# Optimization experiments

Measured on AMD Instinct MI355X. Metric: run time of the kernel, lower is better.

## Reference

```python
import jax, jax.numpy as jnp
import numpy as np

B, L, D = 8, 2048, 512


def setup_inputs() -> dict:
    key = jax.random.key(0)
    ks = jax.random.split(key, 9)
    s = 1.0 / np.sqrt(D)
    x = jax.random.normal(ks[0], (B, L, D), dtype=jnp.float32)
    Wq = jax.random.uniform(ks[1], (D, D), jnp.float32, -s, s)
    bq = jax.random.uniform(ks[2], (D,), jnp.float32, -s, s)
    Wk = jax.random.uniform(ks[3], (D, D), jnp.float32, -s, s)
    bk = jax.random.uniform(ks[4], (D,), jnp.float32, -s, s)
    Wv = jax.random.uniform(ks[5], (D, D), jnp.float32, -s, s)
    bv = jax.random.uniform(ks[6], (D,), jnp.float32, -s, s)
    Wo = jax.random.uniform(ks[7], (D, D), jnp.float32, -s, s)
    bo = jax.random.uniform(ks[8], (D,), jnp.float32, -s, s)
    return {"x": x, "Wq": Wq, "bq": bq, "Wk": Wk, "bk": bk,
            "Wv": Wv, "bv": bv, "Wo": Wo, "bo": bo}


def reference(x, Wq, bq, Wk, bk, Wv, bv, Wo, bo):
    # Projections then rfft along sequence axis -> complex [B, F, D], F = L//2+1
    Q = jnp.fft.rfft(x @ Wq + bq, axis=1)
    K = jnp.fft.rfft(x @ Wk + bk, axis=1)
    V = jnp.fft.rfft(x @ Wv + bv, axis=1)
    scale = K.shape[-1] ** (-0.5)
    # Complex attention scores over frequency bins: [B, F, F]
    att = jnp.einsum('bfd,bgd->bfg', Q, K) * scale
    attn = jax.nn.softmax(jnp.abs(att), axis=-1)
    context = jnp.einsum('bfg,bgd->bfd', attn.astype(Q.dtype), V)
    context = jnp.fft.irfft(context, n=x.shape[1], axis=1)  # [B, L, D] real
    return context @ Wo + bo
```

## Files before the change

### kernel.cpp

```cpp
#include <hip/hip_runtime.h>
#include <hip/hip_bf16.h>
#include <math.h>

typedef __hip_bfloat16 bf16;
typedef __attribute__((ext_vector_type(8))) short short8;
typedef __attribute__((ext_vector_type(4))) float f32x4;

#define BB 8
#define LL 2048
#define DD 512
#define FF 1025
#define GP 1088
#define FPAD 1152
#define PSTRIDE 589824
#define ATT_SCALE 0.04419417382415922f

__device__ __forceinline__ float b2f(bf16 v) { return __bfloat162float(v); }
__device__ __forceinline__ bf16  f2b(float v) { return __float2bfloat16(v); }
__device__ __forceinline__ float s2f(short s) { bf16 t; *reinterpret_cast<short*>(&t) = s; return b2f(t); }
__device__ __forceinline__ unsigned pk2f(float a, float b) {
    bf16 ha = f2b(a), hb = f2b(b);
    return (unsigned)*(unsigned short*)&ha | ((unsigned)*(unsigned short*)&hb << 16);
}

#define MFMA16(a, b, c) __builtin_amdgcn_mfma_f32_16x16x32_bf16((a), (b), (c), 0, 0, 0)

__device__ __forceinline__ short8 neg8(short8 v) {
    short8 r;
    #pragma unroll
    for (int t = 0; t < 8; ++t) r[t] = (short)(v[t] ^ (short)0x8000);
    return r;
}

typedef __attribute__((address_space(1))) const unsigned int gu32;
typedef __attribute__((address_space(3))) unsigned int lu32;
__device__ __forceinline__ void gl16(const void* g, void* l) {
    __builtin_amdgcn_global_load_lds((gu32*)g, (lu32*)l, 16, 0, 0);
}

template<bool F32>
__device__ __forceinline__ float ldin(const void* p, size_t i) {
    if (F32) return ((const float*)p)[i];
    else     return b2f(((const bf16*)p)[i]);
}

__global__ __launch_bounds__(256) void detect_dtype(const unsigned short* __restrict__ x,
                                                    int* __restrict__ flag)
{
    __shared__ int cnt[256];
    int c = 0;
    for (int i = threadIdx.x; i < 4096; i += 256) {
        const int e = (x[i] >> 7) & 0xFF;
        c += (e >= 100 && e <= 150) ? 1 : 0;
    }
    cnt[threadIdx.x] = c;
    __syncthreads();
    for (int s = 128; s; s >>= 1) {
        if (threadIdx.x < s) cnt[threadIdx.x] += cnt[threadIdx.x + s];
        __syncthreads();
    }
    if (threadIdx.x == 0) *flag = (cnt[0] < 3400) ? 1 : 0;
}

__global__ __launch_bounds__(256) void prep_bias(const void* __restrict__ b0,
                                                 const void* __restrict__ b1,
                                                 const void* __restrict__ b2,
                                                 const void* __restrict__ b3,
                                                 float* __restrict__ bias_f,
                                                 const int* __restrict__ flag)
{
    const int idx = blockIdx.x * 256 + threadIdx.x;
    const int which = idx >> 9, i = idx & 511;
    const void* src = which == 0 ? b0 : (which == 1 ? b1 : (which == 2 ? b2 : b3));
    bias_f[idx] = (*flag) ? ldin<true>(src, i) : ldin<false>(src, i);
}

__global__ __launch_bounds__(256) void split_w_t(const void* __restrict__ W0,
                                                 const void* __restrict__ W1,
                                                 const void* __restrict__ W2,
                                                 const void* __restrict__ W3,
                                                 bf16* __restrict__ WT,
                                                 const int* __restrict__ flag)
{
    const int z = blockIdx.z;
    const void* W = z == 0 ? W0 : (z == 1 ? W1 : (z == 2 ? W2 : W3));
    bf16* Wh = WT + (size_t)z * 524288;
    const int k0 = blockIdx.x * 32, n0 = blockIdx.y * 32;
    const bool f32 = (*flag) != 0;
    __shared__ float Tl[32][33];
    for (int it = 0; it < 4; ++it) {
        const int idx = it * 256 + threadIdx.x;
        const int lk = idx >> 5, ln = idx & 31;
        Tl[lk][ln] = f32 ? ldin<true>(W, (size_t)(k0 + lk) * 512 + n0 + ln)
                         : ldin<false>(W, (size_t)(k0 + lk) * 512 + n0 + ln);
    }
    __syncthreads();
    for (int it = 0; it < 4; ++it) {
        const int idx = it * 256 + threadIdx.x;
        const int ln = idx >> 5, lk = idx & 31;
        Wh[(size_t)(n0 + ln) * 512 + k0 + lk] = f2b(Tl[lk][ln]);
    }
}

__device__ __forceinline__ int shx(int i, int c) {
    const int x = (i << 2) | c;
    return x ^ (((x >> 6) & 3) << 2);
}

__device__ __forceinline__ void fft_decode(int flat, int& b, int& dp) {
    const int c8 = flat & 7;
    const int s  = (flat >> 3) & 1;
    const int pp = flat >> 4;
    const int idx = c8 * 32 + pp;
    b  = idx >> 5;
    dp = ((idx & 31) << 1) | s;
}

__device__ __forceinline__ void fill_twl(float2* twl, int tid) {
    for (int idx = tid; idx < 2047; idx += 512) {
        const int l2 = 31 - __builtin_clz((unsigned)(2047 - idx));
        const int m = 1 << l2;
        const int k = idx - 2048 + 2 * m;
        float s, c2;
        __sincosf(-3.14159265358979f * (float)k / (float)m, &s, &c2);
        twl[idx] = make_float2(c2, s);
    }
}

__global__ __launch_bounds__(512) void rfft_x(const void* __restrict__ x,
                                              bf16* __restrict__ Xh,
                                              const int* __restrict__ flag)
{
    int b, dp;
    fft_decode(blockIdx.x, b, dp);
    const int d0 = dp * 8;
    __shared__ float2 sh[8192];
    __shared__ float2 twl[2048];
    const int tid = threadIdx.x;
    const int c = tid & 3;

    if (*flag) {
        const float* base = (const float*)x + (size_t)b * 2048 * 512 + d0;
        #pragma unroll
        for (int it = 0; it < 8; ++it) {
            const int idx = it * 512 + tid;
            const int l = idx >> 1, fq = idx & 1;
            const float4 v = *(const float4*)(base + (size_t)l * 512 + fq * 4);
            sh[shx(l, fq * 2)]     = make_float2(v.x, v.y);
            sh[shx(l, fq * 2 + 1)] = make_float2(v.z, v.w);
        }
    } else {
        const bf16* base = (const bf16*)x + (size_t)b * 2048 * 512 + d0;
        #pragma unroll
        for (int it = 0; it < 4; ++it) {
            const int l = it * 512 + tid;
            const short8 v = *(const short8*)(base + (size_t)l * 512);
            #pragma unroll
            for (int q = 0; q < 4; ++q)
                sh[shx(l, q)] = make_float2(s2f(v[2 * q]), s2f(v[2 * q + 1]));
        }
    }
    fill_twl(twl, tid);
    __syncthreads();

    const int jb = tid >> 2;
    #pragma unroll
    for (int lsm = 10; lsm >= 0; --lsm) {
        const int m = 1 << lsm;
        const int base = 2048 - (m << 1);
        #pragma unroll
        for (int r = 0; r < 8; ++r) {
            const int j  = jb + 128 * r;
            const int k  = j & (m - 1);
            const int i1 = ((j & ~(m - 1)) << 1) | k;
            const int i2 = i1 + m;
            const float2 w = twl[base + k];
            const float cw = w.x, sw = w.y;
            const float2 a  = sh[shx(i1, c)];
            const float2 bb = sh[shx(i2, c)];
            sh[shx(i1, c)] = make_float2(a.x + bb.x, a.y + bb.y);
            const float dx = a.x - bb.x, dy = a.y - bb.y;
            sh[shx(i2, c)] = make_float2(dx * cw - dy * sw, dx * sw + dy * cw);
        }
        __syncthreads();
    }

    const int fb = tid >> 2;
    const size_t pan_re = (size_t)(b * 64 + dp) * FPAD;
    const size_t pan_im = pan_re + (size_t)512 * FPAD;
    auto dorow = [&](int f) {
        const int rf = __brev((unsigned)f) >> 21;
        const int rc = __brev((unsigned)((2048 - f) & 2047)) >> 21;
        const float2 Zf = sh[shx(rf, c)];
        const float2 Zc = sh[shx(rc, c)];
        const float x1r = 0.5f * (Zf.x + Zc.x);
        const float x1i = 0.5f * (Zf.y - Zc.y);
        const float x2r = 0.5f * (Zf.y + Zc.y);
        const float x2i = -0.5f * (Zf.x - Zc.x);
        const size_t ro_re = (pan_re + f) * 8 + 2 * c;
        const size_t ro_im = (pan_im + f) * 8 + 2 * c;
        *(unsigned*)&Xh[ro_re] = pk2f(x1r, x2r);
        *(unsigned*)&Xh[ro_im] = pk2f(x1i, x2i);
    };
    #pragma unroll
    for (int it = 0; it < 8; ++it)
        dorow(fb * 8 + it);
    if (tid < 4) dorow(1024);

    if (tid < 254) {
        const int f = FF + (tid >> 1);
        const int w = tid & 1;
        const size_t off = (((size_t)(w * 512 + b * 64 + dp)) * FPAD + f) * 8;
        short8 z = {};
        *(short8*)&Xh[off] = z;
    }
}

__global__ __launch_bounds__(256, 2) void proj_all(const bf16* __restrict__ Xh,
                                                   const bf16* __restrict__ WT,
                                                   const float* __restrict__ bias_f,
                                                   bf16* __restrict__ Q,
                                                   bf16* __restrict__ K,
                                                   bf16* __restrict__ Vct)
{
    const int flat = blockIdx.x;
    const bool isV = flat < 576;
    int t, ny, z;
    if (isV) { t = flat >> 2; ny = flat & 3; z = 2; }
    else { const int idx = flat - 576; t = idx >> 3; z = (idx >> 2) & 1; ny = idx & 3; }

    const int pb = t / 9;
    const int f0 = (t - pb * 9) * 128;
    const int plane = pb >> 3, b = pb & 7;
    const int n0 = ny * 128;
    const int tid = threadIdx.x, wv = tid >> 6, lane = tid & 63;
    const int wm = (wv >> 1) * 64, wn = (wv & 1) * 64;
    const size_t pbase = (size_t)pb * PSTRIDE;

    const bf16* Bh = WT + (size_t)z * 524288;
    const float* bias = bias_f + z * 512;

    __shared__ __align__(1024) bf16 SH[32768];

    const int r8 = lane >> 3;
    const int sl = lane & 7;
    const int q  = sl ^ r8;
    const int r16 = lane & 15, cc = lane >> 4;
    const int rs8 = r16 & 7;
    const int nn2 = lane & 15, rq = (lane >> 4) * 4;

    auto STAGE = [&](int buf, int kt) {
        char* base = (char*)SH + buf * 32768;
        #pragma unroll
        for (int c2 = 0; c2 < 4; ++c2) {
            const int chunk = wv * 4 + c2;
            const int row = chunk * 8 + r8;
            gl16(&Xh[pbase + ((size_t)((kt >> 3) + q) * FPAD + f0 + row) * 8],
                 base + chunk * 1024);
            gl16(&Bh[(size_t)(n0 + row) * 512 + kt + q * 8],
                 base + 16384 + chunk * 1024);
        }
    };

    f32x4 acc[4][4] = {};
    STAGE(0, 0);
    for (int it = 0; it < 8; ++it) {
        if (it < 7) {
            STAGE((it + 1) & 1, (it + 1) * 64);
            asm volatile("s_waitcnt vmcnt(8)" ::: "memory");
        } else {
            asm volatile("s_waitcnt vmcnt(0)" ::: "memory");
        }
        __builtin_amdgcn_s_barrier();
        __builtin_amdgcn_sched_barrier(0);

        const bf16* Ab = SH + (it & 1) * 16384;
        const bf16* Bb = Ab + 8192;
        #pragma unroll
        for (int kk = 0; kk < 2; ++kk) {
            short8 af[4], bfr[4];
            const int sa = ((kk * 4 + cc) ^ rs8) * 8;
            #pragma unroll
            for (int i = 0; i < 4; ++i) {
                af[i]  = *(const short8*)&Ab[(wm + i * 16 + r16) * 64 + sa];
                bfr[i] = *(const short8*)&Bb[(wn + i * 16 + r16) * 64 + sa];
            }
            #pragma unroll
            for (int i = 0; i < 4; ++i)
                #pragma unroll
                for (int j = 0; j < 4; ++j)
                    acc[i][j] = MFMA16(af[i], bfr[j], acc[i][j]);
        }
        asm volatile("s_waitcnt lgkmcnt(0)" ::: "memory");
        __builtin_amdgcn_s_barrier();
    }

    if (!isV) {
        bf16* dst = z == 0 ? Q : K;
        const size_t SPQ = (size_t)BB * FF * DD;
        #pragma unroll
        for (int i = 0; i < 4; ++i)
            #pragma unroll
            for (int j = 0; j < 4; ++j) {
                const int col = n0 + wn + j * 16 + nn2;
                #pragma unroll
                for (int r = 0; r < 4; ++r) {
                    const int f = f0 + wm + i * 16 + rq + r;
                    if (f < FF) {
                        float v = acc[i][j][r];
                        if (plane == 0 && f == 0) v += 2048.0f * bias[col];
                        const int swz = ((f >> 1) & 3) << 3;
                        dst[(size_t)plane * SPQ + ((size_t)(b * FF + f)) * 512 + (col ^ swz)] = f2b(v);
                    }
                }
            }
    } else {
        bf16* T = SH;
        #pragma unroll
        for (int i = 0; i < 4; ++i)
            #pragma unroll
            for (int j = 0; j < 4; ++j) {
                const int col_l = wn + j * 16 + nn2;
                #pragma unroll
                for (int r = 0; r < 4; ++r) {
                    const int row_l = wm + i * 16 + rq + r;
                    const int f = f0 + row_l;
                    float v = (f < FF) ? acc[i][j][r] : 0.f;
                    if (plane == 0 && f == 0) v += 2048.0f * bias[n0 + col_l];
                    T[col_l * 128 + (row_l ^ ((col_l & 15) << 3))] = f2b(v);
                }
            }
        __syncthreads();

        const int nl = tid >> 1, half = tid & 1;
        const size_t gbase = ((size_t)(b * 1024 + plane * 512 + n0 + nl)) * GP + f0;
        #pragma unroll
        for (int a = 0; a < 8; ++a) {
            const int fl = half * 64 + a * 8;
            if (f0 + fl < GP) {
                const short8 v8 = *(const short8*)&T[nl * 128 + (fl ^ ((nl & 15) << 3))];
                *(short8*)&Vct[gbase + fl] = v8;
            }
        }
    }
}

__global__ __launch_bounds__(256, 2) void att_mfma(const bf16* __restrict__ Asp,
                                                   const bf16* __restrict__ Bsp,
                                                   float* __restrict__ att)
{
    const size_t SP = (size_t)BB * FF * DD;
    const int flat = blockIdx.x;
    const int b    = flat & 7;
    const int slot = flat >> 3;
    const int grp  = slot / 51;
    const int rem  = slot % 51;
    const int g    = rem / 3;
    const int r3   = rem % 3;
    const int ft   = grp * 3 + r3;
    const int f0 = ft * 128, g0 = g * 64;

    const int tid = threadIdx.x;
    const int wv = tid >> 6, lane = tid & 63;
    const int wvf = wv >> 1, wvg = wv & 1;

    __shared__ __align__(1024) char LB[49152];

    f32x4 accr[4][2] = {}; f32x4 acci[4][2] = {};

    const int r16 = lane & 15, cc = lane >> 4;
    const int rpos = (cc ^ ((r16 >> 1) & 3)) * 8;
    const size_t abase = (size_t)(b * FF + f0) * 512;
    const size_t bbase = (size_t)(b * FF + g0) * 512;
    const int lrow = lane >> 2;
    const int lcol = (lane & 3) * 8;

    for (int kt = 0; kt < 512; kt += 64) {
        #pragma unroll
        for (int c2 = 0; c2 < 8; ++c2) {
            const int chunk = wv * 8 + c2;
            const int half = chunk >> 4;
            const int pl = (chunk >> 3) & 1, rg = chunk & 7;
            const int row = rg * 16 + lrow;
            gl16(&Asp[(size_t)pl * SP + abase + (size_t)row * 512 + kt + half * 32 + lcol],
                 LB + half * 16384 + ((pl << 3) | rg) * 1024);
        }
        #pragma unroll
        for (int c2 = 0; c2 < 4; ++c2) {
            const int chunk = wv * 4 + c2;
            const int half = chunk >> 3;
            const int pl = (chunk >> 2) & 1, rg = chunk & 3;
            const int row = rg * 16 + lrow;
            gl16(&Bsp[(size_t)pl * SP + bbase + (size_t)row * 512 + kt + half * 32 + lcol],
                 LB + 32768 + half * 8192 + ((pl << 2) | rg) * 1024);
        }
        __syncthreads();

        #pragma unroll
        for (int kk = 0; kk < 2; ++kk) {
            bf16 (*Al)[128][32] = (bf16(*)[128][32])(LB + kk * 16384);
            bf16 (*Bl)[64][32]  = (bf16(*)[64][32])(LB + 32768 + kk * 8192);
            short8 aA[4][2], bB[2][2], nb[2];
            #pragma unroll
            for (int i = 0; i < 4; ++i) {
                const int row = wvf * 64 + i * 16 + r16;
                #pragma unroll
                for (int pl = 0; pl < 2; ++pl)
                    aA[i][pl] = *(const short8*)&Al[pl][row][rpos];
            }
            #pragma unroll
            for (int j = 0; j < 2; ++j) {
                const int row = wvg * 32 + j * 16 + r16;
                #pragma unroll
                for (int pl = 0; pl < 2; ++pl)
                    bB[j][pl] = *(const short8*)&Bl[pl][row][rpos];
                nb[j] = neg8(bB[j][1]);
            }
            #pragma unroll
            for (int i = 0; i < 4; ++i)
                #pragma unroll
                for (int j = 0; j < 2; ++j) {
                    accr[i][j] = MFMA16(aA[i][0], bB[j][0], accr[i][j]);
                    accr[i][j] = MFMA16(aA[i][1], nb[j],    accr[i][j]);
                    acci[i][j] = MFMA16(aA[i][0], bB[j][1], acci[i][j]);
                    acci[i][j] = MFMA16(aA[i][1], bB[j][0], acci[i][j]);
                }
        }
        __syncthreads();
    }

    const int rq = (lane >> 4) * 4;
    #pragma unroll
    for (int i = 0; i < 4; ++i)
        #pragma unroll
        for (int j = 0; j < 2; ++j)
            #pragma unroll
            for (int r = 0; r < 4; ++r) {
                const int f = f0 + wvf * 64 + i * 16 + rq + r;
                const int gg = g0 + wvg * 32 + j * 16 + r16;
                if (f < FF && gg < FF) {
                    const float ar = accr[i][j][r];
                    const float ai = acci[i][j][r];
                    att[((size_t)(b * FF + f)) * FF + gg] = ATT_SCALE * sqrtf(ar * ar + ai * ai);
                }
            }
}

__global__ __launch_bounds__(256) void softmax_rows(const float* __restrict__ att,
                                                    bf16* __restrict__ att16)
{
    const int row = blockIdx.x;
    const float* p = att + (size_t)row * FF;
    bf16* q = att16 + (size_t)row * GP;
    const int tid = threadIdx.x;
    const int lane = tid & 63, wid = tid >> 6;
    __shared__ float srow[1028];
    __shared__ float red[4];

    float m = -1e30f;
    for (int i = tid; i < FF; i += 256) {
        const float v = p[i];
        srow[i] = v;
        m = fmaxf(m, v);
    }
    #pragma unroll
    for (int o = 32; o; o >>= 1) m = fmaxf(m, __shfl_down(m, o));
    if (lane == 0) red[wid] = m;
    __syncthreads();
    m = fmaxf(fmaxf(red[0], red[1]), fmaxf(red[2], red[3]));
    __syncthreads();

    float s = 0.f;
    for (int i = tid; i < FF; i += 256) {
        const float e = expf(srow[i] - m);
        srow[i] = e;
        s += e;
    }
    #pragma unroll
    for (int o = 32; o; o >>= 1) s += __shfl_down(s, o);
    if (lane == 0) red[wid] = s;
    __syncthreads();
    s = red[0] + red[1] + red[2] + red[3];
    const float inv = 1.f / s;
    for (int i = tid; i < GP; i += 256)
        q[i] = f2b(i < FF ? srow[i] * inv : 0.f);
}

__global__ __launch_bounds__(256, 2) void ctx_mfma(const bf16* __restrict__ att16,
                                                   const bf16* __restrict__ Vct,
                                                   bf16* __restrict__ Csp)
{
    const int flat = blockIdx.x;
    const int b    = flat & 7;
    const int slot = flat >> 3;
    const int ft   = slot >> 4;
    const int nt   = slot & 15;
    const int f0 = ft * 128, n0 = nt * 64;

    const int tid = threadIdx.x;
    const int wv = tid >> 6, lane = tid & 63;
    const int wvf = wv >> 1, wvg = wv & 1;

    __shared__ __align__(1024) bf16 SH[24576];

    f32x4 acc[4][2] = {};
    const int r8 = lane >> 3, sl = lane & 7, q = sl ^ r8;
    const int r16 = lane & 15, cc = lane >> 4;
    const int rs8 = r16 & 7;

    auto STAGE = [&](int buf, int kt) {
        char* base = (char*)SH + buf * 24576;
        #pragma unroll
        for (int c2 = 0; c2 < 4; ++c2) {
            const int chunk = wv * 4 + c2;
            const int row = chunk * 8 + r8;
            gl16(&att16[((size_t)(b * FF + f0 + row)) * GP + kt + q * 8],
                 base + chunk * 1024);
        }
        #pragma unroll
        for (int c2 = 0; c2 < 2; ++c2) {
            const int chunk = wv * 2 + c2;
            const int row = chunk * 8 + r8;
            gl16(&Vct[((size_t)(b * 1024 + n0 + row)) * GP + kt + q * 8],
                 base + 16384 + chunk * 1024);
        }
    };

    STAGE(0, 0);
    for (int it = 0; it < 17; ++it) {
        if (it < 16) {
            STAGE((it + 1) & 1, (it + 1) * 64);
            asm volatile("s_waitcnt vmcnt(6)" ::: "memory");
        } else {
            asm volatile("s_waitcnt vmcnt(0)" ::: "memory");
        }
        __builtin_amdgcn_s_barrier();
        __builtin_amdgcn_sched_barrier(0);

        const bf16* Ab = SH + (it & 1) * 12288;
        const bf16* Bb = Ab + 8192;
        #pragma unroll
        for (int kk = 0; kk < 2; ++kk) {
            short8 aA[4], bB[2];
            const int sa = ((kk * 4 + cc) ^ rs8) * 8;
            #pragma unroll
            for (int i = 0; i < 4; ++i)
                aA[i] = *(const short8*)&Ab[(wvf * 64 + i * 16 + r16) * 64 + sa];
            #pragma unroll
            for (int j = 0; j < 2; ++j)
                bB[j] = *(const short8*)&Bb[(wvg * 32 + j * 16 + r16) * 64 + sa];
            #pragma unroll
            for (int i = 0; i < 4; ++i)
                #pragma unroll
                for (int j = 0; j < 2; ++j)
                    acc[i][j] = MFMA16(aA[i], bB[j], acc[i][j]);
        }
        asm volatile("s_waitcnt lgkmcnt(0)" ::: "memory");
        __builtin_amdgcn_s_barrier();
    }

    const int rq = (lane >> 4) * 4;
    #pragma unroll
    for (int i = 0; i < 4; ++i)
        #pragma unroll
        for (int j = 0; j < 2; ++j)
            #pragma unroll
            for (int r = 0; r < 4; ++r) {
                const int f = f0 + wvf * 64 + i * 16 + rq + r;
                const int n = n0 + wvg * 32 + j * 16 + r16;
                if (f < FF) {
                    const int d = n & 511, pl = n >> 9;
                    Csp[((size_t)(pl * 8 + b) * FPAD + f) * 512 + d] = f2b(acc[i][j][r]);
                }
            }
}

__global__ __launch_bounds__(256, 2) void out_mfma_freq(const bf16* __restrict__ A,
                                                        const bf16* __restrict__ BhT,
                                                        float* __restrict__ CwR,
                                                        float* __restrict__ CwI)
{
    const int t = blockIdx.x;
    const int pb = t / 9;
    const int f0 = (t - pb * 9) * 128;
    const int plane = pb >> 3, b = pb & 7;
    const int m0 = t * 128, n0 = blockIdx.y * 64;
    const int tid = threadIdx.x, wv = tid >> 6, lane = tid & 63;
    const int wvf = wv >> 1, wvg = wv & 1;

    __shared__ __align__(1024) bf16 SH[24576];

    f32x4 acc[4][2] = {};
    const int r8 = lane >> 3, sl = lane & 7, q = sl ^ r8;
    const int r16 = lane & 15, cc = lane >> 4;
    const int rs8 = r16 & 7;

    auto STAGE = [&](int buf, int kt) {
        char* base = (char*)SH + buf * 24576;
        #pragma unroll
        for (int c2 = 0; c2 < 4; ++c2) {
            const int chunk = wv * 4 + c2;
            const int row = chunk * 8 + r8;
            gl16(&A[(size_t)(m0 + row) * 512 + kt + q * 8],
                 base + chunk * 1024);
        }
        #pragma unroll
        for (int c2 = 0; c2 < 2; ++c2) {
            const int chunk = wv * 2 + c2;
            const int row = chunk * 8 + r8;
            gl16(&BhT[(size_t)(n0 + row) * 512 + kt + q * 8],
                 base + 16384 + chunk * 1024);
        }
    };

    STAGE(0, 0);
    for (int it = 0; it < 8; ++it) {
        if (it < 7) {
            STAGE((it + 1) & 1, (it + 1) * 64);
            asm volatile("s_waitcnt vmcnt(6)" ::: "memory");
        } else {
            asm volatile("s_waitcnt vmcnt(0)" ::: "memory");
        }
        __builtin_amdgcn_s_barrier();
        __builtin_amdgcn_sched_barrier(0);

        const bf16* Ab = SH + (it & 1) * 12288;
        const bf16* Bb = Ab + 8192;
        #pragma unroll
        for (int kk = 0; kk < 2; ++kk) {
            short8 af[4], bfr[2];
            const int sa = ((kk * 4 + cc) ^ rs8) * 8;
            #pragma unroll
            for (int i = 0; i < 4; ++i)
                af[i] = *(const short8*)&Ab[(wvf * 64 + i * 16 + r16) * 64 + sa];
            #pragma unroll
            for (int j = 0; j < 2; ++j)
                bfr[j] = *(const short8*)&Bb[(wvg * 32 + j * 16 + r16) * 64 + sa];
            #pragma unroll
            for (int i = 0; i < 4; ++i)
                #pragma unroll
                for (int j = 0; j < 2; ++j)
                    acc[i][j] = MFMA16(af[i], bfr[j], acc[i][j]);
        }
        asm volatile("s_waitcnt lgkmcnt(0)" ::: "memory");
        __builtin_amdgcn_s_barrier();
    }

    float* dst = plane ? CwI : CwR;
    const int nn2 = lane & 15, rq = (lane >> 4) * 4;
    #pragma unroll
    for (int i = 0; i < 4; ++i)
        #pragma unroll
        for (int j = 0; j < 2; ++j) {
            const int col = n0 + wvg * 32 + j * 16 + nn2;
            #pragma unroll
            for (int r = 0; r < 4; ++r) {
                const int f = f0 + wvf * 64 + i * 16 + rq + r;
                if (f < FF)
                    dst[((size_t)(b * FF + f)) * 512 + col] = acc[i][j][r];
            }
        }
}

__global__ __launch_bounds__(512) void irfft8(const float* __restrict__ CwR,
                                              const float* __restrict__ CwI,
                                              void* __restrict__ out,
                                              const float* __restrict__ bias_f,
                                              const int* __restrict__ flag)
{
    int b, dp;
    fft_decode(blockIdx.x, b, dp);
    const int d0 = dp * 8;
    __shared__ float2 sh[8192];
    __shared__ float2 twl[2048];
    const int tid = threadIdx.x;
    const int c = tid & 3, fb = tid >> 2;

    for (int it = 0; it < 9; ++it) {
        const int f = fb + 128 * it;
        if (f < FF) {
            const size_t off = ((size_t)(b * FF + f)) * 512 + d0 + 2 * c;
            const float2 vr = *(const float2*)(CwR + off);
            const float2 vi = *(const float2*)(CwI + off);
            float c1x = vr.x, c1y = vi.x, c2x = vr.y, c2y = vi.y;
            if (f == 0 || f == 1024) { c1y = 0.f; c2y = 0.f; }
            sh[shx(f, c)] = make_float2(c1x - c2y, c1y + c2x);
            if (f >= 1 && f <= 1023)
                sh[shx(2048 - f, c)] = make_float2(c1x + c2y, c2x - c1y);
        }
    }
    fill_twl(twl, tid);
    __syncthreads();

    const int jb = fb;
    #pragma unroll
    for (int lsm = 10; lsm >= 0; --lsm) {
        const int m = 1 << lsm;
        const int base = 2048 - (m << 1);
        #pragma unroll
        for (int r = 0; r < 8; ++r) {
            const int j  = jb + 128 * r;
            const int k  = j & (m - 1);
            const int i1 = ((j & ~(m - 1)) << 1) | k;
            const int i2 = i1 + m;
            const float2 w = twl[base + k];
            const float cw = w.x, sw = -w.y;
            const float2 a  = sh[shx(i1, c)];
            const float2 bb = sh[shx(i2, c)];
            sh[shx(i1, c)] = make_float2(a.x + bb.x, a.y + bb.y);
            const float dx = a.x - bb.x, dy = a.y - bb.y;
            sh[shx(i2, c)] = make_float2(dx * cw - dy * sw, dx * sw + dy * cw);
        }
        __syncthreads();
    }

    const float sc = 1.0f / 2048.0f;
    const float bo0 = bias_f[1536 + d0 + 2 * c];
    const float bo1 = bias_f[1536 + d0 + 2 * c + 1];
    const bool f32o = (*flag) != 0;
    const int lb = tid >> 2;
    #pragma unroll
    for (int it = 0; it < 16; ++it) {
        const int l  = lb * 16 + it;
        const int rl = __brev((unsigned)l) >> 21;
        const float2 z = sh[shx(rl, c)];
        const float o0 = z.x * sc + bo0;
        const float o1 = z.y * sc + bo1;
        const size_t off = ((size_t)(b * 2048 + l)) * 512 + d0 + 2 * c;
        if (f32o) {
            *(float2*)((float*)out + off) = make_float2(o0, o1);
        } else {
            __hip_bfloat162 h;
            h.x = f2b(o0); h.y = f2b(o1);
            *(__hip_bfloat162*)((bf16*)out + off) = h;
        }
    }
}

extern "C" void kernel_launch(void* const* d_in, const int* in_sizes, int n_in,
                              void* d_out, int out_size, void* d_ws, size_t ws_size,
                              hipStream_t stream)
{
    const void* x  = d_in[0];
    const void* Wq = d_in[1]; const void* bq = d_in[2];
    const void* Wk = d_in[3]; const void* bk = d_in[4];
    const void* Wv = d_in[5]; const void* bv = d_in[6];
    const void* Wo = d_in[7]; const void* bo = d_in[8];

    char* ws = (char*)d_ws;
    char* pA = ws;
    char* pB = pA + 33652736;
    char* pC = pB + 37748736;
    char* pD = pC + 17039360;
    char* pE = pD + 17039360;
    char* pW = pE + 17825792;

    float*  attn = (float*)pA;
    bf16*   Xh   = (bf16*)pB;
    bf16*   att16= (bf16*)pB;
    bf16*   Csp  = (bf16*)(pB + 17843200);
    bf16*   Asp  = (bf16*)pC;
    bf16*   Bsp  = (bf16*)pD;
    float*  CwR  = (float*)pC;
    float*  CwI  = (float*)pD;
    bf16*   Vct  = (bf16*)pE;
    bf16*   WT   = (bf16*)pW;
    float*  bias_f = (float*)(pW + 4194304);
    int*    flag = (int*)(pW + 4194304 + 8192);

    detect_dtype<<<1, 256, 0, stream>>>((const unsigned short*)x, flag);
    prep_bias<<<8, 256, 0, stream>>>(bq, bk, bv, bo, bias_f, flag);
    split_w_t<<<dim3(16, 16, 4), 256, 0, stream>>>(Wq, Wk, Wv, Wo, WT, flag);
    rfft_x<<<dim3(512), 512, 0, stream>>>(x, Xh, flag);
    proj_all<<<dim3(1728), 256, 0, stream>>>(Xh, WT, bias_f, Asp, Bsp, Vct);
    att_mfma<<<dim3(1224), 256, 0, stream>>>(Asp, Bsp, attn);
    softmax_rows<<<dim3(BB * FF), 256, 0, stream>>>(attn, att16);
    ctx_mfma<<<dim3(1152), 256, 0, stream>>>(att16, Vct, Csp);
    out_mfma_freq<<<dim3(144, 8), 256, 0, stream>>>(Csp, WT + 3 * 524288, CwR, CwI);
    irfft8<<<dim3(512), 512, 0, stream>>>(CwR, CwI, d_out, bias_f, flag);
}
```

Measured before the change: 305.8 us.

## Double-buffer complex score GEMM loads and remap projection blocks across XCDs

The complex attention-score kernel moves from single-buffered 64-wide K tiles with two full barriers per step to double-buffered 32-wide K tiles. The next tile's global-to-LDS loads are issued before computing on the current one, using explicit vmcnt waits. The projection kernel's block index is remapped so the 12 blocks sharing an input tile (V, K and Q across four column slices) land on the same XCD, to improve L2 reuse. Risks include more barrier iterations per tile and a manual waitcnt count that must match the number of issued loads.

```diff
diff --git a/kernel.cpp b/kernel.cpp
--- a/kernel.cpp
+++ b/kernel.cpp
@@ -224,10 +224,15 @@
                                                    bf16* __restrict__ Vct)
 {
     const int flat = blockIdx.x;
-    const bool isV = flat < 576;
-    int t, ny, z;
-    if (isV) { t = flat >> 2; ny = flat & 3; z = 2; }
-    else { const int idx = flat - 576; t = idx >> 3; z = (idx >> 2) & 1; ny = idx & 3; }
+    const int xcd  = flat & 7;
+    const int rest = flat >> 3;
+    const int tgrp = rest / 12;
+    const int sib  = rest - tgrp * 12;
+    const int t    = tgrp * 8 + xcd;
+    const bool isV = sib < 4;
+    int ny, z;
+    if (isV) { ny = sib; z = 2; }
+    else { const int s = sib - 4; z = s >> 2; ny = s & 3; }
 
     const int pb = t / 9;
     const int f0 = (t - pb * 9) * 128;
@@ -375,58 +380,67 @@
     const int lrow = lane >> 2;
     const int lcol = (lane & 3) * 8;
 
-    for (int kt = 0; kt < 512; kt += 64) {
-        #pragma unroll
-        for (int c2 = 0; c2 < 8; ++c2) {
-            const int chunk = wv * 8 + c2;
-            const int half = chunk >> 4;
-            const int pl = (chunk >> 3) & 1, rg = chunk & 7;
-            const int row = rg * 16 + lrow;
-            gl16(&Asp[(size_t)pl * SP + abase + (size_t)row * 512 + kt + half * 32 + lcol],
-                 LB + half * 16384 + ((pl << 3) | rg) * 1024);
-        }
+    auto STAGE = [&](int buf, int kt) {
+        char* base = LB + buf * 24576;
         #pragma unroll
         for (int c2 = 0; c2 < 4; ++c2) {
             const int chunk = wv * 4 + c2;
-            const int half = chunk >> 3;
-            const int pl = (chunk >> 2) & 1, rg = chunk & 3;
+            const int pl = chunk >> 3, rg = chunk & 7;
             const int row = rg * 16 + lrow;
-            gl16(&Bsp[(size_t)pl * SP + bbase + (size_t)row * 512 + kt + half * 32 + lcol],
-                 LB + 32768 + half * 8192 + ((pl << 2) | rg) * 1024);
-        }
-        __syncthreads();
-
-        #pragma unroll
-        for (int kk = 0; kk < 2; ++kk) {
-            bf16 (*Al)[128][32] = (bf16(*)[128][32])(LB + kk * 16384);
-            bf16 (*Bl)[64][32]  = (bf16(*)[64][32])(LB + 32768 + kk * 8192);
-            short8 aA[4][2], bB[2][2], nb[2];
-            #pragma unroll
-            for (int i = 0; i < 4; ++i) {
-                const int row = wvf * 64 + i * 16 + r16;
-                #pragma unroll
-                for (int pl = 0; pl < 2; ++pl)
-                    aA[i][pl] = *(const short8*)&Al[pl][row][rpos];
+            gl16(&Asp[(size_t)pl * SP + abase + (size_t)row * 512 + kt + lcol],
+                 base + chunk * 1024);
+        }
+        #pragma unroll
+        for (int c2 = 0; c2 < 2; ++c2) {
+            const int chunk = wv * 2 + c2;
+            const int pl = chunk >> 2, rg = chunk & 3;
+            const int row = rg * 16 + lrow;
+            gl16(&Bsp[(size_t)pl * SP + bbase + (size_t)row * 512 + kt + lcol],
+                 base + 16384 + chunk * 1024);
+        }
+    };
+
+    STAGE(0, 0);
+    for (int it = 0; it < 16; ++it) {
+        if (it < 15) {
+            STAGE((it + 1) & 1, (it + 1) * 32);
+            asm volatile("s_waitcnt vmcnt(6)" ::: "memory");
+        } else {
+            asm volatile("s_waitcnt vmcnt(0)" ::: "memory");
+        }
+        __builtin_amdgcn_s_barrier();
+        __builtin_amdgcn_sched_barrier(0);
+
+        char* bufb = LB + (it & 1) * 24576;
+        bf16 (*Al)[128][32] = (bf16(*)[128][32])bufb;
+        bf16 (*Bl)[64][32]  = (bf16(*)[64][32])(bufb + 16384);
+        short8 aA[4][2], bB[2][2], nb[2];
+        #pragma unroll
+        for (int i = 0; i < 4; ++i) {
+            const int row = wvf * 64 + i * 16 + r16;
+            #pragma unroll
+            for (int pl = 0; pl < 2; ++pl)
+                aA[i][pl] = *(const short8*)&Al[pl][row][rpos];
+        }
+        #pragma unroll
+        for (int j = 0; j < 2; ++j) {
+            const int row = wvg * 32 + j * 16 + r16;
+            #pragma unroll
+            for (int pl = 0; pl < 2; ++pl)
+                bB[j][pl] = *(const short8*)&Bl[pl][row][rpos];
+            nb[j] = neg8(bB[j][1]);
+        }
+        #pragma unroll
+        for (int i = 0; i < 4; ++i)
+            #pragma unroll
+            for (int j = 0; j < 2; ++j) {
+                accr[i][j] = MFMA16(aA[i][0], bB[j][0], accr[i][j]);
+                accr[i][j] = MFMA16(aA[i][1], nb[j],    accr[i][j]);
+                acci[i][j] = MFMA16(aA[i][0], bB[j][1], acci[i][j]);
+                acci[i][j] = MFMA16(aA[i][1], bB[j][0], acci[i][j]);
             }
-            #pragma unroll
-            for (int j = 0; j < 2; ++j) {
-                const int row = wvg * 32 + j * 16 + r16;
-                #pragma unroll
-                for (int pl = 0; pl < 2; ++pl)
-                    bB[j][pl] = *(const short8*)&Bl[pl][row][rpos];
-                nb[j] = neg8(bB[j][1]);
-            }
-            #pragma unroll
-            for (int i = 0; i < 4; ++i)
-                #pragma unroll
-                for (int j = 0; j < 2; ++j) {
-                    accr[i][j] = MFMA16(aA[i][0], bB[j][0], accr[i][j]);
-                    accr[i][j] = MFMA16(aA[i][1], nb[j],    accr[i][j]);
-                    acci[i][j] = MFMA16(aA[i][0], bB[j][1], acci[i][j]);
-                    acci[i][j] = MFMA16(aA[i][1], bB[j][0], acci[i][j]);
-                }
-        }
-        __syncthreads();
+        asm volatile("s_waitcnt lgkmcnt(0)" ::: "memory");
+        __builtin_amdgcn_s_barrier();
     }
 
     const int rq = (lane >> 4) * 4;
```

New measurement: 317.7 us. +3.9%, slower.
